# Kernel optimization log

Measured on AMD Instinct MI355X. Metric: run time of the kernel, lower is better.

Reference implementation:

```python
import jax, jax.numpy as jnp
import numpy as np

L, D, N_HEADS = 4096, 1024, 16
HEAD_D = D // N_HEADS


def setup_inputs() -> dict:
    key = jax.random.key(0)
    kx, kq, kbq, ko, kbo = jax.random.split(key, 5)
    lim_in = 1.0 / np.sqrt(D)
    return {
        "x": jax.random.normal(kx, (L, D), dtype=jnp.float32),
        # equinox nn.Linear(dim, 3*dim): weight [3D, D], bias [3D], uniform(-1/sqrt(in), 1/sqrt(in))
        "W_qkv": jax.random.uniform(kq, (3 * D, D), jnp.float32, -lim_in, lim_in),
        "b_qkv": jax.random.uniform(kbq, (3 * D,), jnp.float32, -lim_in, lim_in),
        "W_out": jax.random.uniform(ko, (D, D), jnp.float32, -lim_in, lim_in),
        "b_out": jax.random.uniform(kbo, (D,), jnp.float32, -lim_in, lim_in),
    }


def reference(x, W_qkv, b_qkv, W_out, b_out):
    # qkv projection: equinox Linear computes W @ x + b per token -> x @ W.T + b
    qkv = x @ W_qkv.T + b_qkv                         # [L, 3D]
    qkv = qkv.reshape(L, 3, N_HEADS, HEAD_D)
    qkv = jnp.transpose(qkv, (1, 2, 0, 3))            # [3, n, L, d]
    q, k, v = qkv[0], qkv[1], qkv[2]                  # each [n, L, d]

    scale = 1.0 / jnp.sqrt(jnp.asarray(HEAD_D, dtype=x.dtype))
    attn = jnp.einsum('nqd,nkd->nqk', q, k) * scale   # [n, L, L]
    causal = jnp.tril(jnp.ones((L, L), dtype=bool))
    attn = jnp.where(causal, attn, -jnp.inf)
    attn = jax.nn.softmax(attn, axis=-1)              # dropout rate 0 -> identity
    out = jnp.einsum('nqk,nkd->nqd', attn, v)         # [n, L, d]
    out = jnp.transpose(out, (1, 0, 2)).reshape(L, D)
    return out @ W_out.T + b_out                      # [L, D]
```

## Files before the change

### kernel.cpp

```cpp
#include <hip/hip_runtime.h>
#include <hip/hip_bf16.h>
#include <math.h>

#define L_SEQ 4096
#define DIM   1024
#define NH    16
#define HD    64

#define QSCL 0.18033688011112042f

typedef __attribute__((ext_vector_type(4)))  float f32x4;
typedef __attribute__((ext_vector_type(16))) float f32x16;
typedef __attribute__((ext_vector_type(8)))  short s16x8;
typedef __attribute__((ext_vector_type(4)))  short s16x4;
typedef __attribute__((ext_vector_type(4)))  unsigned u32x4;

__device__ __forceinline__ short f2bf(float f) {
  unsigned u = __builtin_bit_cast(unsigned, f);
  u = u + 0x7fffu + ((u >> 16) & 1u);
  return (short)(u >> 16);
}

__device__ __forceinline__ unsigned cvt_pk_bf16(float lo, float hi_) {
  unsigned r;
  asm("v_cvt_pk_bf16_f32 %0, %1, %2" : "=v"(r) : "v"(lo), "v"(hi_));
  return r;
}

__device__ __forceinline__ float exp2_fast(float x) {
  float r;
  asm("v_exp_f32 %0, %1" : "=v"(r) : "v"(x));
  return r;
}

__device__ __forceinline__ void gload_lds16(const void* g, void* l) {
  __builtin_amdgcn_global_load_lds(
      (__attribute__((address_space(1))) void*)(g),
      (__attribute__((address_space(3))) void*)(l), 16, 0, 0);
}

__global__ __launch_bounds__(256) void cvt_f32_bf16(const float* __restrict__ src,
                                                    short* __restrict__ dst, int n4) {
  int i = blockIdx.x * 256 + threadIdx.x;
  if (i >= n4) return;
  f32x4 f = *(const f32x4*)(src + i * 4);
  s16x4 o;
  o[0] = f2bf(f[0]); o[1] = f2bf(f[1]); o[2] = f2bf(f[2]); o[3] = f2bf(f[3]);
  *(s16x4*)(dst + i * 4) = o;
}


#define GEMM_MAINLOOP(A_, B_, Kdim)                                            \
  f32x4 acc[4][4];                                                             \
  _Pragma("unroll") for (int m = 0; m < 4; ++m)                                \
  _Pragma("unroll") for (int n = 0; n < 4; ++n) acc[m][n] = (f32x4)0.f;        \
  const short* aptr = A_ + (bm * 128 + w * 16 + (l >> 2)) * (Kdim) + (l & 3) * 8; \
  const short* bptr = B_ + (bn * 128 + w * 16 + (l >> 2)) * (Kdim) + (l & 3) * 8; \
  short* asl = &As[(w * 16) * 32];                                             \
  short* bsl = &Bs[(w * 16) * 32];                                             \
  for (int kk = 0; kk < (Kdim); kk += 32) {                                    \
    gload_lds16(aptr + kk, asl);                                               \
    gload_lds16(aptr + kk + 64 * (Kdim), asl + 64 * 32);                       \
    gload_lds16(bptr + kk, bsl);                                               \
    gload_lds16(bptr + kk + 64 * (Kdim), bsl + 64 * 32);                       \
    __syncthreads();                                                           \
    s16x8 af[4], bfr[4];                                                       \
    _Pragma("unroll") for (int m = 0; m < 4; ++m)                              \
      af[m] = *(const s16x8*)&As[(wr * 64 + m * 16 + lr) * 32 + lg * 8];       \
    _Pragma("unroll") for (int n = 0; n < 4; ++n)                              \
      bfr[n] = *(const s16x8*)&Bs[(wc * 64 + n * 16 + lr) * 32 + lg * 8];      \
    _Pragma("unroll") for (int m = 0; m < 4; ++m)                              \
    _Pragma("unroll") for (int n = 0; n < 4; ++n)                              \
      acc[m][n] = __builtin_amdgcn_mfma_f32_16x16x32_bf16(af[m], bfr[n], acc[m][n], 0, 0, 0); \
    __syncthreads();                                                           \
  }

__global__ __launch_bounds__(256) void gemm_qkv(const short* __restrict__ A,
                                                const short* __restrict__ B,
                                                const float* __restrict__ bias,
                                                short* __restrict__ Qb,
                                                short* __restrict__ Kf,
                                                short* __restrict__ Vf) {
  __shared__ __align__(16) short As[128 * 32];
  __shared__ __align__(16) short Bs[128 * 32];
  const int t = threadIdx.x;
  const int w = t >> 6, l = t & 63;
  const int wr = w >> 1, wc = w & 1;
  const int lr = l & 15, lg = l >> 4;
  const int bm = blockIdx.x, bn = blockIdx.y;

  GEMM_MAINLOOP(A, B, DIM)

  const int row0 = bm * 128 + wr * 64;
  const int col0 = bn * 128 + wc * 64;
#pragma unroll
  for (int n = 0; n < 4; ++n) {
    const int col = col0 + n * 16 + lr;
    const float bv = bias[col];
    const int which = col >> 10;
    const int head = (col & 1023) >> 6;
    const int d = col & 63;
    if (which == 0) {
      short* dst = Qb + (head * L_SEQ) * HD + d;
#pragma unroll
      for (int m = 0; m < 4; ++m)
#pragma unroll
        for (int j = 0; j < 4; ++j) {
          const int row = row0 + m * 16 + lg * 4 + j;
          dst[row * HD] = f2bf((acc[m][n][j] + bv) * QSCL);
        }
    } else if (which == 1) {
      const int c = d >> 4, khi = (d >> 3) & 1, e = d & 7;
      short* dst = Kf + head * (L_SEQ * HD);
#pragma unroll
      for (int m = 0; m < 4; ++m)
#pragma unroll
        for (int j = 0; j < 4; ++j) {
          const int row = row0 + m * 16 + lg * 4 + j;
          const int p = row >> 5;
          const int lane = khi * 32 + (row & 31);
          dst[((p * 4 + c) * 64 + lane) * 8 + e] = f2bf(acc[m][n][j] + bv);
        }
    } else {
      const int dh = d >> 5;
      const int dq = d & 31;
      short* dst = Vf + head * (L_SEQ * HD);
#pragma unroll
      for (int m = 0; m < 4; ++m) {
        const int rowb = row0 + m * 16 + lg * 4;
        const int tt = rowb >> 6;
        const int kc = (rowb >> 4) & 3;
        const int khi = (rowb >> 3) & 1;
        const int e0 = rowb & 7;
        s16x4 wv;
#pragma unroll
        for (int j = 0; j < 4; ++j) wv[j] = f2bf(acc[m][n][j] + bv);
        *(s16x4*)&dst[(((tt * 4 + kc) * 2 + dh) * 64 + khi * 32 + dq) * 8 + e0] = wv;
      }
    }
  }
}

__global__ __launch_bounds__(256) void gemm_out(const short* __restrict__ A,
                                                const short* __restrict__ B,
                                                const float* __restrict__ bias,
                                                float* __restrict__ C) {
  __shared__ __align__(16) short As[128 * 32];
  __shared__ __align__(16) short Bs[128 * 32];
  const int t = threadIdx.x;
  const int w = t >> 6, l = t & 63;
  const int wr = w >> 1, wc = w & 1;
  const int lr = l & 15, lg = l >> 4;
  const int bm = blockIdx.x, bn = blockIdx.y;

  GEMM_MAINLOOP(A, B, DIM)

  const int row0 = bm * 128 + wr * 64;
  const int col0 = bn * 128 + wc * 64;
#pragma unroll
  for (int n = 0; n < 4; ++n) {
    const int col = col0 + n * 16 + lr;
    const float bv = bias[col];
#pragma unroll
    for (int m = 0; m < 4; ++m)
#pragma unroll
      for (int j = 0; j < 4; ++j) {
        const int row = row0 + m * 16 + lg * 4 + j;
        C[row * DIM + col] = acc[m][n][j] + bv;
      }
  }
}

__global__ __launch_bounds__(128, 4) void attn32(const short* __restrict__ Qb,
                                                 const short* __restrict__ Kf,
                                                 const short* __restrict__ Vf,
                                                 short* __restrict__ Ob) {
  __shared__ float Mg[64 * 33];
  const int bid = blockIdx.x;
  const int xcd = bid & 7;
  const int idx = bid >> 3;
  const int head = (xcd << 1) | (idx & 1);
  const int qt = idx >> 1;
  const int qtile = (qt & 1) ? (qt >> 1) : (127 - (qt >> 1));
  const int q0 = qtile * 32;
  const int h = threadIdx.x >> 6;
  const int l = threadIdx.x & 63;
  const int q = l & 31;
  const int hi = l >> 5;

  const short* Qh = Qb + head * (L_SEQ * HD);
  const short* Kh = Kf + head * (L_SEQ * HD);
  const short* Vh = Vf + head * (L_SEQ * HD);

  s16x8 qf[4];
#pragma unroll
  for (int c = 0; c < 4; ++c)
    qf[c] = *(const s16x8*)&Qh[(q0 + q) * HD + c * 16 + hi * 8];

  f32x16 o0 = (f32x16)0.f, o1 = (f32x16)0.f;
  f32x4 lvec = (f32x4)0.f;

  const int nkt = qtile + 1;

  s16x8 kf[4];
#pragma unroll
  for (int c = 0; c < 4; ++c)
    kf[c] = *(const s16x8*)&Kh[((h * 4 + c) * 64 + l) * 8];

  for (int kt = h; kt < nkt; kt += 2) {
    s16x8 vf[2][2];
#pragma unroll
    for (int cc = 0; cc < 2; ++cc)
#pragma unroll
      for (int dh = 0; dh < 2; ++dh)
        vf[cc][dh] = *(const s16x8*)
            &Vh[((((kt >> 1) * 4 + (kt & 1) * 2 + cc) * 2 + dh) * 64 + l) * 8];

    f32x16 s = (f32x16)0.f;
#pragma unroll
    for (int c = 0; c < 4; ++c)
      s = __builtin_amdgcn_mfma_f32_32x32x16_bf16(kf[c], qf[c], s, 0, 0, 0);

    const int ktn = (kt + 2 < nkt) ? kt + 2 : kt;
#pragma unroll
    for (int c = 0; c < 4; ++c)
      kf[c] = *(const s16x8*)&Kh[((ktn * 4 + c) * 64 + l) * 8];

    if (kt == qtile) {
      const int qrel = q - hi * 4;
#pragma unroll
      for (int r = 0; r < 16; ++r) {
        const int koff = (r & 3) + 8 * (r >> 2);
        if (koff > qrel) s[r] = -1e30f;
      }
    }

#pragma unroll
    for (int r = 0; r < 16; ++r) s[r] = exp2_fast(s[r]);
#pragma unroll
    for (int r = 0; r < 16; ++r) lvec[r & 3] += s[r];

#pragma unroll
    for (int cc = 0; cc < 2; ++cc) {
      const int roff = cc * 8;
      const unsigned A = cvt_pk_bf16(s[roff + 0], s[roff + 1]);
      const unsigned B = cvt_pk_bf16(s[roff + 2], s[roff + 3]);
      const unsigned C = cvt_pk_bf16(s[roff + 4], s[roff + 5]);
      const unsigned D = cvt_pk_bf16(s[roff + 6], s[roff + 7]);
      const unsigned sA = (unsigned)__shfl_xor((int)A, 32, 64);
      const unsigned sB = (unsigned)__shfl_xor((int)B, 32, 64);
      const unsigned sC = (unsigned)__shfl_xor((int)C, 32, 64);
      const unsigned sD = (unsigned)__shfl_xor((int)D, 32, 64);
      u32x4 pw;
      pw[0] = hi ? sC : A;
      pw[1] = hi ? sD : B;
      pw[2] = hi ? C : sA;
      pw[3] = hi ? D : sB;
      const s16x8 pf = __builtin_bit_cast(s16x8, pw);
      o0 = __builtin_amdgcn_mfma_f32_32x32x16_bf16(vf[cc][0], pf, o0, 0, 0, 0);
      o1 = __builtin_amdgcn_mfma_f32_32x32x16_bf16(vf[cc][1], pf, o1, 0, 0, 0);
    }
  }

  float lsum = (lvec[0] + lvec[1]) + (lvec[2] + lvec[3]);
  lsum += __shfl_xor(lsum, 32, 64);

  if (h == 0) {
    float* st = &Mg[l * 33];
    st[0] = lsum;
#pragma unroll
    for (int r = 0; r < 16; ++r) { st[1 + r] = o0[r]; st[17 + r] = o1[r]; }
  }
  __syncthreads();
  if (h == 1) {
    const float* st = &Mg[l * 33];
    const float inv = 1.f / (st[0] + lsum);
    const int orow = q0 + q;
#pragma unroll
    for (int dh = 0; dh < 2; ++dh) {
#pragma unroll
      for (int tq = 0; tq < 4; ++tq) {
        s16x4 wv;
#pragma unroll
        for (int j = 0; j < 4; ++j) {
          const int r = tq * 4 + j;
          const float ov = (dh == 0) ? (st[1 + r] + o0[r]) : (st[17 + r] + o1[r]);
          wv[j] = f2bf(ov * inv);
        }
        *(s16x4*)&Ob[orow * DIM + head * HD + dh * 32 + tq * 8 + hi * 4] = wv;
      }
    }
  }
}

extern "C" void kernel_launch(void* const* d_in, const int* in_sizes, int n_in,
                              void* d_out, int out_size, void* d_ws, size_t ws_size,
                              hipStream_t stream) {
  const float* x    = (const float*)d_in[0];
  const float* Wqkv = (const float*)d_in[1];
  const float* bqkv = (const float*)d_in[2];
  const float* Wout = (const float*)d_in[3];
  const float* bout = (const float*)d_in[4];
  float* out = (float*)d_out;

  char* ws = (char*)d_ws;
  short* xb    = (short*)(ws);
  short* wqkvb = (short*)(ws + (8u  << 20));
  short* woutb = (short*)(ws + (14u << 20));
  short* Qb    = (short*)(ws + (16u << 20));
  short* Kf    = (short*)(ws + (24u << 20));
  short* Vf    = (short*)(ws + (32u << 20));
  short* Ob    = (short*)(ws + (40u << 20));

  cvt_f32_bf16<<<(L_SEQ * DIM / 4 + 255) / 256, 256, 0, stream>>>(x, xb, L_SEQ * DIM / 4);
  cvt_f32_bf16<<<(3 * DIM * DIM / 4 + 255) / 256, 256, 0, stream>>>(Wqkv, wqkvb, 3 * DIM * DIM / 4);
  cvt_f32_bf16<<<(DIM * DIM / 4 + 255) / 256, 256, 0, stream>>>(Wout, woutb, DIM * DIM / 4);

  gemm_qkv<<<dim3(L_SEQ / 128, 3 * DIM / 128), 256, 0, stream>>>(xb, wqkvb, bqkv, Qb, Kf, Vf);
  attn32<<<2048, 128, 0, stream>>>(Qb, Kf, Vf, Ob);
  gemm_out<<<dim3(L_SEQ / 128, DIM / 128), 256, 0, stream>>>(Ob, woutb, bout, out);
}
```

Measured before the change: 144.5 us.

## Merge bf16 conversion launches and shrink output GEMM tile to 64x64

Folds the three f32-to-bf16 conversion launches into a single kernel that picks its source and destination by global index, which removes two launch overheads. It also replaces the 128x128-tile output projection GEMM with a 64x64-tile variant, raising the grid from 256 to 1024 blocks so all CUs have work. The trade-off is less operand reuse per tile, fewer MFMAs between barriers, and more redundant global and L2 traffic for A and B.

Result: faster. 137.9 us (-4.6%).

```diff
diff --git a/kernel.cpp b/kernel.cpp
--- a/kernel.cpp
+++ b/kernel.cpp
@@ -39,14 +39,27 @@
       (__attribute__((address_space(3))) void*)(l), 16, 0, 0);
 }
 
-__global__ __launch_bounds__(256) void cvt_f32_bf16(const float* __restrict__ src,
-                                                    short* __restrict__ dst, int n4) {
+#define CVT_N1 (L_SEQ * DIM / 4)
+#define CVT_N2 (3 * DIM * DIM / 4)
+#define CVT_N3 (DIM * DIM / 4)
+
+__global__ __launch_bounds__(256) void cvt_all(const float* __restrict__ x,
+                                               const float* __restrict__ Wqkv,
+                                               const float* __restrict__ Wout,
+                                               short* __restrict__ xb,
+                                               short* __restrict__ wqkvb,
+                                               short* __restrict__ woutb) {
   int i = blockIdx.x * 256 + threadIdx.x;
-  if (i >= n4) return;
-  f32x4 f = *(const f32x4*)(src + i * 4);
+  const float* src;
+  short* dst;
+  int j;
+  if (i < CVT_N1)               { src = x;    dst = xb;    j = i; }
+  else if (i < CVT_N1 + CVT_N2) { src = Wqkv; dst = wqkvb; j = i - CVT_N1; }
+  else                          { src = Wout; dst = woutb; j = i - CVT_N1 - CVT_N2; }
+  f32x4 f = *(const f32x4*)(src + j * 4);
   s16x4 o;
   o[0] = f2bf(f[0]); o[1] = f2bf(f[1]); o[2] = f2bf(f[2]); o[3] = f2bf(f[3]);
-  *(s16x4*)(dst + i * 4) = o;
+  *(s16x4*)(dst + j * 4) = o;
 }
 
 
@@ -141,28 +154,56 @@
   }
 }
 
-__global__ __launch_bounds__(256) void gemm_out(const short* __restrict__ A,
-                                                const short* __restrict__ B,
-                                                const float* __restrict__ bias,
-                                                float* __restrict__ C) {
-  __shared__ __align__(16) short As[128 * 32];
-  __shared__ __align__(16) short Bs[128 * 32];
+__global__ __launch_bounds__(256) void gemm_out64(const short* __restrict__ A,
+                                                  const short* __restrict__ B,
+                                                  const float* __restrict__ bias,
+                                                  float* __restrict__ C) {
+  __shared__ __align__(16) short As[64 * 32];
+  __shared__ __align__(16) short Bs[64 * 32];
   const int t = threadIdx.x;
   const int w = t >> 6, l = t & 63;
   const int wr = w >> 1, wc = w & 1;
   const int lr = l & 15, lg = l >> 4;
   const int bm = blockIdx.x, bn = blockIdx.y;
 
-  GEMM_MAINLOOP(A, B, DIM)
-
-  const int row0 = bm * 128 + wr * 64;
-  const int col0 = bn * 128 + wc * 64;
-#pragma unroll
-  for (int n = 0; n < 4; ++n) {
+  f32x4 acc[2][2];
+#pragma unroll
+  for (int m = 0; m < 2; ++m)
+#pragma unroll
+    for (int n = 0; n < 2; ++n) acc[m][n] = (f32x4)0.f;
+
+  const short* aptr = A + (bm * 64 + (t >> 2)) * DIM + (t & 3) * 8;
+  const short* bptr = B + (bn * 64 + (t >> 2)) * DIM + (t & 3) * 8;
+  short* asl = &As[t * 8];
+  short* bsl = &Bs[t * 8];
+
+  for (int kk = 0; kk < DIM; kk += 32) {
+    gload_lds16(aptr + kk, asl);
+    gload_lds16(bptr + kk, bsl);
+    __syncthreads();
+    s16x8 af[2], bfr[2];
+#pragma unroll
+    for (int m = 0; m < 2; ++m)
+      af[m] = *(const s16x8*)&As[(wr * 32 + m * 16 + lr) * 32 + lg * 8];
+#pragma unroll
+    for (int n = 0; n < 2; ++n)
+      bfr[n] = *(const s16x8*)&Bs[(wc * 32 + n * 16 + lr) * 32 + lg * 8];
+#pragma unroll
+    for (int m = 0; m < 2; ++m)
+#pragma unroll
+      for (int n = 0; n < 2; ++n)
+        acc[m][n] = __builtin_amdgcn_mfma_f32_16x16x32_bf16(af[m], bfr[n], acc[m][n], 0, 0, 0);
+    __syncthreads();
+  }
+
+  const int row0 = bm * 64 + wr * 32;
+  const int col0 = bn * 64 + wc * 32;
+#pragma unroll
+  for (int n = 0; n < 2; ++n) {
     const int col = col0 + n * 16 + lr;
     const float bv = bias[col];
 #pragma unroll
-    for (int m = 0; m < 4; ++m)
+    for (int m = 0; m < 2; ++m)
 #pragma unroll
       for (int j = 0; j < 4; ++j) {
         const int row = row0 + m * 16 + lg * 4 + j;
@@ -312,11 +353,9 @@
   short* Vf    = (short*)(ws + (32u << 20));
   short* Ob    = (short*)(ws + (40u << 20));
 
-  cvt_f32_bf16<<<(L_SEQ * DIM / 4 + 255) / 256, 256, 0, stream>>>(x, xb, L_SEQ * DIM / 4);
-  cvt_f32_bf16<<<(3 * DIM * DIM / 4 + 255) / 256, 256, 0, stream>>>(Wqkv, wqkvb, 3 * DIM * DIM / 4);
-  cvt_f32_bf16<<<(DIM * DIM / 4 + 255) / 256, 256, 0, stream>>>(Wout, woutb, DIM * DIM / 4);
+  cvt_all<<<(CVT_N1 + CVT_N2 + CVT_N3) / 256, 256, 0, stream>>>(x, Wqkv, Wout, xb, wqkvb, woutb);
 
   gemm_qkv<<<dim3(L_SEQ / 128, 3 * DIM / 128), 256, 0, stream>>>(xb, wqkvb, bqkv, Qb, Kf, Vf);
   attn32<<<2048, 128, 0, stream>>>(Qb, Kf, Vf, Ob);
-  gemm_out<<<dim3(L_SEQ / 128, DIM / 128), 256, 0, stream>>>(Ob, woutb, bout, out);
-}
+  gemm_out64<<<dim3(L_SEQ / 64, DIM / 64), 256, 0, stream>>>(Ob, woutb, bout, out);
+}
```
